# Optimization experiments

Measured on AMD Instinct MI355X. Metric: run time of the kernel, lower is better.

## Reference

```python
import jax, jax.numpy as jnp
import numpy as np

# Model config (matches init_kwargs)
B, S = 4, 1024          # batch of equal-length prefill sequences (cu_seqlens = arange(B+1)*S)
H, KVH, D = 16, 4, 64   # query heads, kv heads (GQA), head_dim
SCALE = 0.125           # 1/sqrt(head_dim)
NUM_SLOTS = 8192        # paged-KV-cache total slots


def setup_inputs() -> dict:
    key = jax.random.key(0)
    k1, k2, k3 = jax.random.split(key, 3)
    N = B * S
    q = jax.random.normal(k1, (N, H * D), dtype=jnp.float32)
    k = jax.random.normal(k2, (N, KVH * D), dtype=jnp.float32)
    v = jax.random.normal(k3, (N, KVH * D), dtype=jnp.float32)
    k_cache = jnp.zeros((NUM_SLOTS, KVH * D), dtype=jnp.float32)
    v_cache = jnp.zeros((NUM_SLOTS, KVH * D), dtype=jnp.float32)
    slot_mapping = jnp.arange(N, dtype=jnp.int32)  # valid slots, no -1 entries
    return {"q": q, "k": k, "v": v, "k_cache": k_cache, "v_cache": v_cache,
            "slot_mapping": slot_mapping}


def _varlen_causal_attn(q, k, v):
    # q: [N, H*D], k/v: [N, KVH*D]; equal-length varlen batch -> [B, S, ...]
    qh = q.reshape(B, S, H, D)
    kh = k.reshape(B, S, KVH, D)
    vh = v.reshape(B, S, KVH, D)
    rep = H // KVH  # GQA: repeat kv heads to match query heads
    kh = jnp.repeat(kh, rep, axis=2)
    vh = jnp.repeat(vh, rep, axis=2)
    scores = jnp.einsum('bqhd,bkhd->bhqk', qh, kh) * SCALE
    causal = jnp.tril(jnp.ones((S, S), dtype=bool))
    scores = jnp.where(causal, scores, jnp.finfo(scores.dtype).min)
    p = jax.nn.softmax(scores, axis=-1)
    o = jnp.einsum('bhqk,bkhd->bqhd', p, vh)
    return o.reshape(B * S, H * D)


def reference(q, k, v, k_cache, v_cache, slot_mapping):
    # store_kvcache: scatter new k/v rows into the paged caches (Triton kernel equivalent)
    k_cache = k_cache.at[slot_mapping].set(k)
    v_cache = v_cache.at[slot_mapping].set(v)
    # prefill path: flash_attn_varlen_func(q, k, v, causal=True) on the fresh k/v
    o = _varlen_causal_attn(q, k, v)
    return o, k_cache, v_cache
```

## Files before the change

kernel.cpp:

```cpp
#include <hip/hip_runtime.h>
#include <hip/hip_bf16.h>

#define B_     4
#define S_     1024
#define H_     16
#define KVH_   4
#define D_     64
#define N_     (B_*S_)
#define SLOTS_ 8192
#define KVD_   (KVH_*D_)
#define HD_    (H_*D_)
#define SCL    (0.125f * 1.44269504f)

#define NATT   1024
#define NCACHE 4096

typedef __attribute__((ext_vector_type(8))) short bf16x8;
typedef __attribute__((ext_vector_type(4))) short bf16x4;
typedef __attribute__((ext_vector_type(4))) float f32x4;

__device__ __forceinline__ short4 f4tob4(float4 f){
    union { __hip_bfloat162 h[2]; short4 s; } u;
    u.h[0] = __float22bfloat162_rn(make_float2(f.x, f.y));
    u.h[1] = __float22bfloat162_rn(make_float2(f.z, f.w));
    return u.s;
}
__device__ __forceinline__ int swz(int row, int col){
    return row*64 + (col ^ ((row & 7) << 3));
}

__global__ void inv_init(int* __restrict__ inv){
    inv[blockIdx.x*256 + threadIdx.x] = -1;
}

__global__ __launch_bounds__(256) void prep_kernel(
    const float* __restrict__ k, const float* __restrict__ v,
    const int* __restrict__ slot_map, int* __restrict__ inv,
    short* __restrict__ Kb, short* __restrict__ Vtb)
{
    const int tid = threadIdx.x;
    if (blockIdx.x >= 256){
        int i = (blockIdx.x - 256)*256 + tid;
        int s = slot_map[i];
        if (s >= 0 && s < SLOTS_) inv[s] = i;
        return;
    }
    __shared__ short sv[64*68];
    const int g   = blockIdx.x >> 4;
    const int s0  = (blockIdx.x & 15) * 64;
    const int b   = g >> 2, kvh = g & 3;

    const int sl = tid >> 2;
    const int cq = (tid & 3) * 16;

    const int n   = b*S_ + s0 + sl;
    const float4* kp = (const float4*)(k + (size_t)n*KVD_ + kvh*D_ + cq);
    const float4* vp = (const float4*)(v + (size_t)n*KVD_ + kvh*D_ + cq);

    float4 kk[4], vv[4];
    #pragma unroll
    for (int j = 0; j < 4; ++j){ kk[j] = kp[j]; vv[j] = vp[j]; }

    short* kbp = Kb + ((size_t)g*S_ + s0 + sl)*64 + cq;
    #pragma unroll
    for (int j = 0; j < 4; ++j)
        *(short4*)(kbp + j*4) = f4tob4(kk[j]);

    #pragma unroll
    for (int j = 0; j < 4; ++j)
        *(short4*)(&sv[sl*68 + cq + j*4]) = f4tob4(vv[j]);
    __syncthreads();

    const int d  = tid >> 2;
    const int sg = (tid & 3) * 16;
    union { short s[16]; bf16x8 v8[2]; } out;
    #pragma unroll
    for (int i = 0; i < 16; ++i)
        out.s[i] = sv[(sg + i)*68 + d];
    short* vtp = Vtb + ((size_t)g*64 + d)*S_ + s0 + sg;
    *(bf16x8*)(vtp)     = out.v8[0];
    *(bf16x8*)(vtp + 8) = out.v8[1];
}

__global__ __launch_bounds__(128, 2) void fused_kernel(
    const float* __restrict__ q, const short* __restrict__ Kb,
    const short* __restrict__ Vtb, float* __restrict__ o,
    const float4* __restrict__ kin, const float4* __restrict__ vin,
    const float4* __restrict__ kcin, const float4* __restrict__ vcin,
    const int* __restrict__ inv,
    float4* __restrict__ kc, float4* __restrict__ vc)
{
    const int tid = threadIdx.x;
    const int bid = blockIdx.x;

    if (bid >= NATT){
        int i = (bid - NATT)*128 + tid;
        int row = i >> 6;
        int n = inv[row];
        if (n >= 0){
            int c = i & 63;
            kc[i] = kin[(size_t)n*64 + c];
            vc[i] = vin[(size_t)n*64 + c];
        } else {
            kc[i] = kcin[i];
            vc[i] = vcin[i];
        }
        return;
    }

    __shared__ __align__(16) short sK[2][64*64];
    __shared__ __align__(16) short sV[2][64*64];

    const int wave = tid >> 6;
    const int lane = tid & 63;
    const int quad = lane >> 4;
    const int l16  = lane & 15;

    const int hp = bid & 1;
    const int g  = (bid >> 1) & 15;
    const int p  = bid >> 5;
    const int qtA = p, qtB = 63 - p;
    const int ntA = (qtA >> 2) + 1;
    const int ntB = (qtB >> 2) + 1;

    const int b = g >> 2, kvh = g & 3;
    const int h = kvh*4 + hp*2 + wave;

    bf16x8 qfA[2], qfB[2];
    {
        const float* qpA = q + ((size_t)(b*S_ + qtA*16 + l16))*HD_ + h*D_ + quad*8;
        const float* qpB = q + ((size_t)(b*S_ + qtB*16 + l16))*HD_ + h*D_ + quad*8;
        #pragma unroll
        for (int ks = 0; ks < 2; ++ks){
            float4 a0 = *(const float4*)(qpA + ks*32);
            float4 a1 = *(const float4*)(qpA + ks*32 + 4);
            float4 b0 = *(const float4*)(qpB + ks*32);
            float4 b1 = *(const float4*)(qpB + ks*32 + 4);
            a0.x*=SCL; a0.y*=SCL; a0.z*=SCL; a0.w*=SCL;
            a1.x*=SCL; a1.y*=SCL; a1.z*=SCL; a1.w*=SCL;
            b0.x*=SCL; b0.y*=SCL; b0.z*=SCL; b0.w*=SCL;
            b1.x*=SCL; b1.y*=SCL; b1.z*=SCL; b1.w*=SCL;
            union { short4 s[2]; bf16x8 v8; } ua, ub;
            ua.s[0] = f4tob4(a0); ua.s[1] = f4tob4(a1);
            ub.s[0] = f4tob4(b0); ub.s[1] = f4tob4(b1);
            qfA[ks] = ua.v8; qfB[ks] = ub.v8;
        }
    }

    f32x4 ofA[4], ofB[4];
    #pragma unroll
    for (int f2 = 0; f2 < 4; ++f2){
        ofA[f2] = (f32x4){0.f,0.f,0.f,0.f};
        ofB[f2] = (f32x4){0.f,0.f,0.f,0.f};
    }
    float lsA = 0.f, lsB = 0.f;
    const int qrowA = qtA*16 + l16, qrowB = qtB*16 + l16;

    const short* Kg = Kb  + (size_t)g*S_*64;
    const short* Vg = Vtb + (size_t)g*64*S_;

    const int rs = tid >> 1;
    const int ch = (tid & 1) * 32;

    bf16x8 kst[4], vst[4];
    #pragma unroll
    for (int j = 0; j < 4; ++j){
        kst[j] = *(const bf16x8*)(Kg + (size_t)rs*64 + ch + j*8);
        vst[j] = *(const bf16x8*)(Vg + (size_t)rs*S_ + ch + j*8);
    }

    for (int t = 0; t < ntB; ++t){
        short* K_ = (short*)sK[t & 1];
        short* V_ = (short*)sV[t & 1];
        #pragma unroll
        for (int j = 0; j < 4; ++j){
            *(bf16x8*)(&K_[swz(rs, ch + j*8)]) = kst[j];
            *(bf16x8*)(&V_[swz(rs, ch + j*8)]) = vst[j];
        }
        if (t + 1 < ntB){
            #pragma unroll
            for (int j = 0; j < 4; ++j){
                kst[j] = *(const bf16x8*)(Kg + (size_t)((t+1)*64 + rs)*64 + ch + j*8);
                vst[j] = *(const bf16x8*)(Vg + (size_t)rs*S_ + (t+1)*64 + ch + j*8);
            }
        }
        __syncthreads();

        const bool actA = (t < ntA);

        bf16x8 kf[2][4];
        #pragma unroll
        for (int ks = 0; ks < 2; ++ks)
            #pragma unroll
            for (int f = 0; f < 4; ++f)
                kf[ks][f] = *(const bf16x8*)(&K_[swz(f*16 + l16, ks*32 + quad*8)]);

        f32x4 scB[4], scA[4];
        #pragma unroll
        for (int f = 0; f < 4; ++f){
            scB[f] = (f32x4){0.f,0.f,0.f,0.f};
            scA[f] = (f32x4){0.f,0.f,0.f,0.f};
        }
        #pragma unroll
        for (int ks = 0; ks < 2; ++ks)
            #pragma unroll
            for (int f = 0; f < 4; ++f)
                scB[f] = __builtin_amdgcn_mfma_f32_16x16x32_bf16(kf[ks][f], qfB[ks], scB[f], 0, 0, 0);
        if (actA){
            #pragma unroll
            for (int ks = 0; ks < 2; ++ks)
                #pragma unroll
                for (int f = 0; f < 4; ++f)
                    scA[f] = __builtin_amdgcn_mfma_f32_16x16x32_bf16(kf[ks][f], qfA[ks], scA[f], 0, 0, 0);
        }

        bf16x4 pfB[4], pfA[4];
        #pragma unroll
        for (int f = 0; f < 4; ++f){
            float4 pf;
            #pragma unroll
            for (int r = 0; r < 4; ++r){
                float pe = __builtin_amdgcn_exp2f(scB[f][r]);
                if (t == ntB - 1 && (t*64 + f*16 + quad*4 + r > qrowB)) pe = 0.f;
                lsB += pe;
                ((float*)&pf)[r] = pe;
            }
            union { short4 s; bf16x4 bv; } u; u.s = f4tob4(pf);
            pfB[f] = u.bv;
        }
        if (actA){
            #pragma unroll
            for (int f = 0; f < 4; ++f){
                float4 pf;
                #pragma unroll
                for (int r = 0; r < 4; ++r){
                    float pe = __builtin_amdgcn_exp2f(scA[f][r]);
                    if (t == ntA - 1 && (t*64 + f*16 + quad*4 + r > qrowA)) pe = 0.f;
                    lsA += pe;
                    ((float*)&pf)[r] = pe;
                }
                union { short4 s; bf16x4 bv; } u; u.s = f4tob4(pf);
                pfA[f] = u.bv;
            }
        }

        #pragma unroll
        for (int f = 0; f < 4; ++f){
            #pragma unroll
            for (int f2 = 0; f2 < 4; ++f2){
                bf16x4 vf = *(const bf16x4*)(&V_[swz(f2*16 + l16, f*16 + quad*4)]);
                ofB[f2] = __builtin_amdgcn_mfma_f32_16x16x16bf16_1k(pfB[f], vf, ofB[f2], 0, 0, 0);
                if (actA)
                    ofA[f2] = __builtin_amdgcn_mfma_f32_16x16x16bf16_1k(pfA[f], vf, ofA[f2], 0, 0, 0);
            }
        }
    }

    auto epilogue = [&](f32x4* of, float lsum, int qt){
        lsum += __shfl_xor(lsum, 16);
        lsum += __shfl_xor(lsum, 32);
        float linv[4];
        #pragma unroll
        for (int r = 0; r < 4; ++r)
            linv[r] = 1.f / __shfl(lsum, quad*4 + r);
        #pragma unroll
        for (int f2 = 0; f2 < 4; ++f2){
            #pragma unroll
            for (int r = 0; r < 4; ++r){
                const int row = qt*16 + quad*4 + r;
                o[((size_t)(b*S_ + row))*HD_ + h*D_ + f2*16 + l16] = of[f2][r] * linv[r];
            }
        }
    };
    epilogue(ofA, lsA, qtA);
    epilogue(ofB, lsB, qtB);
}

extern "C" void kernel_launch(void* const* d_in, const int* in_sizes, int n_in,
                              void* d_out, int out_size, void* d_ws, size_t ws_size,
                              hipStream_t stream){
    (void)in_sizes; (void)n_in; (void)out_size; (void)ws_size;
    const float* q     = (const float*)d_in[0];
    const float* k     = (const float*)d_in[1];
    const float* v     = (const float*)d_in[2];
    const float* kc_in = (const float*)d_in[3];
    const float* vc_in = (const float*)d_in[4];
    const int*   slot  = (const int*)d_in[5];

    float* o  = (float*)d_out;
    float* kc = o + (size_t)N_*HD_;
    float* vc = kc + (size_t)SLOTS_*KVD_;

    short* Kb  = (short*)d_ws;
    short* Vt  = Kb + (size_t)16*S_*64;
    int*   inv = (int*)((char*)d_ws + (4u << 20));

    inv_init<<<SLOTS_/256, 256, 0, stream>>>(inv);

    prep_kernel<<<256 + N_/256, 256, 0, stream>>>(k, v, slot, inv, Kb, Vt);

    fused_kernel<<<NATT + NCACHE, 128, 0, stream>>>(
        q, Kb, Vt, o,
        (const float4*)k, (const float4*)v,
        (const float4*)kc_in, (const float4*)vc_in, inv,
        (float4*)kc, (float4*)vc);
}
```

Baseline: 123.4 us.

## Process two query heads per wave and split cache fill into separate kernel

Each attention wave now handles two query heads of the same GQA group. That halves the attention grid to 512 blocks and doubles reuse of each K/V tile loaded into shared memory. The cache scatter-copy work moves out of the fused kernel into its own launch with 256-thread blocks. This trades fewer blocks and more registers per wave, which risks lower occupancy and fewer blocks than CUs, plus serialising the cache copy behind attention, for halved K/V shared-memory traffic per head.

```diff
diff --git a/kernel.cpp b/kernel.cpp
--- a/kernel.cpp
+++ b/kernel.cpp
@@ -11,9 +11,6 @@
 #define KVD_   (KVH_*D_)
 #define HD_    (H_*D_)
 #define SCL    (0.125f * 1.44269504f)
-
-#define NATT   1024
-#define NCACHE 4096
 
 typedef __attribute__((ext_vector_type(8))) short bf16x8;
 typedef __attribute__((ext_vector_type(4))) short bf16x4;
@@ -82,198 +79,184 @@
     *(bf16x8*)(vtp + 8) = out.v8[1];
 }
 
-__global__ __launch_bounds__(128, 2) void fused_kernel(
+__global__ __launch_bounds__(128, 2) void attn_kernel(
     const float* __restrict__ q, const short* __restrict__ Kb,
-    const short* __restrict__ Vtb, float* __restrict__ o,
+    const short* __restrict__ Vtb, float* __restrict__ o)
+{
+    __shared__ __align__(16) short sK[2][64*64];
+    __shared__ __align__(16) short sV[2][64*64];
+
+    const int tid  = threadIdx.x;
+    const int wave = tid >> 6;
+    const int lane = tid & 63;
+    const int quad = lane >> 4;
+    const int l16  = lane & 15;
+
+    const int g = blockIdx.x & 15;
+    const int p = blockIdx.x >> 4;
+    const int qtA = p, qtB = 63 - p;
+    const int ntA = (qtA >> 2) + 1;
+    const int ntB = (qtB >> 2) + 1;
+
+    const int b = g >> 2, kvh = g & 3;
+    const int h0 = kvh*4 + wave*2;
+
+    bf16x8 qfA[2][2], qfB[2][2];
+    auto load_q = [&](int qt, int h, bf16x8 out[2]){
+        const float* qp = q + ((size_t)(b*S_ + qt*16 + l16))*HD_ + h*D_ + quad*8;
+        #pragma unroll
+        for (int ks = 0; ks < 2; ++ks){
+            float4 a0 = *(const float4*)(qp + ks*32);
+            float4 a1 = *(const float4*)(qp + ks*32 + 4);
+            a0.x*=SCL; a0.y*=SCL; a0.z*=SCL; a0.w*=SCL;
+            a1.x*=SCL; a1.y*=SCL; a1.z*=SCL; a1.w*=SCL;
+            union { short4 s[2]; bf16x8 v8; } u;
+            u.s[0] = f4tob4(a0); u.s[1] = f4tob4(a1);
+            out[ks] = u.v8;
+        }
+    };
+    load_q(qtA, h0,   qfA[0]);
+    load_q(qtA, h0+1, qfA[1]);
+    load_q(qtB, h0,   qfB[0]);
+    load_q(qtB, h0+1, qfB[1]);
+
+    f32x4 ofA[2][4], ofB[2][4];
+    float lsA[2] = {0.f, 0.f}, lsB[2] = {0.f, 0.f};
+    #pragma unroll
+    for (int hh = 0; hh < 2; ++hh)
+        #pragma unroll
+        for (int f2 = 0; f2 < 4; ++f2){
+            ofA[hh][f2] = (f32x4){0.f,0.f,0.f,0.f};
+            ofB[hh][f2] = (f32x4){0.f,0.f,0.f,0.f};
+        }
+    const int qrowA = qtA*16 + l16, qrowB = qtB*16 + l16;
+
+    const short* Kg = Kb  + (size_t)g*S_*64;
+    const short* Vg = Vtb + (size_t)g*64*S_;
+
+    const int rs = tid >> 1;
+    const int ch = (tid & 1) * 32;
+
+    bf16x8 kst[4], vst[4];
+    #pragma unroll
+    for (int j = 0; j < 4; ++j){
+        kst[j] = *(const bf16x8*)(Kg + (size_t)rs*64 + ch + j*8);
+        vst[j] = *(const bf16x8*)(Vg + (size_t)rs*S_ + ch + j*8);
+    }
+
+    for (int t = 0; t < ntB; ++t){
+        short* K_ = (short*)sK[t & 1];
+        short* V_ = (short*)sV[t & 1];
+        #pragma unroll
+        for (int j = 0; j < 4; ++j){
+            *(bf16x8*)(&K_[swz(rs, ch + j*8)]) = kst[j];
+            *(bf16x8*)(&V_[swz(rs, ch + j*8)]) = vst[j];
+        }
+        if (t + 1 < ntB){
+            #pragma unroll
+            for (int j = 0; j < 4; ++j){
+                kst[j] = *(const bf16x8*)(Kg + (size_t)((t+1)*64 + rs)*64 + ch + j*8);
+                vst[j] = *(const bf16x8*)(Vg + (size_t)rs*S_ + (t+1)*64 + ch + j*8);
+            }
+        }
+        __syncthreads();
+
+        const bool actA = (t < ntA);
+
+        bf16x8 kf[2][4];
+        #pragma unroll
+        for (int ks = 0; ks < 2; ++ks)
+            #pragma unroll
+            for (int f = 0; f < 4; ++f)
+                kf[ks][f] = *(const bf16x8*)(&K_[swz(f*16 + l16, ks*32 + quad*8)]);
+
+        auto stream_qk = [&](const bf16x8 qf2[2], float& lsum, bool diag,
+                             int qrow, bf16x4 pf_out[4]){
+            f32x4 sc[4];
+            #pragma unroll
+            for (int f = 0; f < 4; ++f) sc[f] = (f32x4){0.f,0.f,0.f,0.f};
+            #pragma unroll
+            for (int ks = 0; ks < 2; ++ks)
+                #pragma unroll
+                for (int f = 0; f < 4; ++f)
+                    sc[f] = __builtin_amdgcn_mfma_f32_16x16x32_bf16(kf[ks][f], qf2[ks], sc[f], 0, 0, 0);
+            #pragma unroll
+            for (int f = 0; f < 4; ++f){
+                float4 pf;
+                #pragma unroll
+                for (int r = 0; r < 4; ++r){
+                    float pe = __builtin_amdgcn_exp2f(sc[f][r]);
+                    if (diag && (t*64 + f*16 + quad*4 + r > qrow)) pe = 0.f;
+                    lsum += pe;
+                    ((float*)&pf)[r] = pe;
+                }
+                union { short4 s; bf16x4 bv; } u; u.s = f4tob4(pf);
+                pf_out[f] = u.bv;
+            }
+        };
+
+        bf16x4 pB[2][4], pA[2][4];
+        stream_qk(qfB[0], lsB[0], t == ntB - 1, qrowB, pB[0]);
+        stream_qk(qfB[1], lsB[1], t == ntB - 1, qrowB, pB[1]);
+        if (actA){
+            stream_qk(qfA[0], lsA[0], t == ntA - 1, qrowA, pA[0]);
+            stream_qk(qfA[1], lsA[1], t == ntA - 1, qrowA, pA[1]);
+        }
+
+        #pragma unroll
+        for (int f = 0; f < 4; ++f){
+            #pragma unroll
+            for (int f2 = 0; f2 < 4; ++f2){
+                bf16x4 vf = *(const bf16x4*)(&V_[swz(f2*16 + l16, f*16 + quad*4)]);
+                ofB[0][f2] = __builtin_amdgcn_mfma_f32_16x16x16bf16_1k(pB[0][f], vf, ofB[0][f2], 0, 0, 0);
+                ofB[1][f2] = __builtin_amdgcn_mfma_f32_16x16x16bf16_1k(pB[1][f], vf, ofB[1][f2], 0, 0, 0);
+                if (actA){
+                    ofA[0][f2] = __builtin_amdgcn_mfma_f32_16x16x16bf16_1k(pA[0][f], vf, ofA[0][f2], 0, 0, 0);
+                    ofA[1][f2] = __builtin_amdgcn_mfma_f32_16x16x16bf16_1k(pA[1][f], vf, ofA[1][f2], 0, 0, 0);
+                }
+            }
+        }
+    }
+
+    auto epilogue = [&](f32x4* of, float lsum, int qt, int h){
+        lsum += __shfl_xor(lsum, 16);
+        lsum += __shfl_xor(lsum, 32);
+        float linv[4];
+        #pragma unroll
+        for (int r = 0; r < 4; ++r)
+            linv[r] = 1.f / __shfl(lsum, quad*4 + r);
+        #pragma unroll
+        for (int f2 = 0; f2 < 4; ++f2){
+            #pragma unroll
+            for (int r = 0; r < 4; ++r){
+                const int row = qt*16 + quad*4 + r;
+                o[((size_t)(b*S_ + row))*HD_ + h*D_ + f2*16 + l16] = of[f2][r] * linv[r];
+            }
+        }
+    };
+    epilogue(ofA[0], lsA[0], qtA, h0);
+    epilogue(ofA[1], lsA[1], qtA, h0+1);
+    epilogue(ofB[0], lsB[0], qtB, h0);
+    epilogue(ofB[1], lsB[1], qtB, h0+1);
+}
+
+__global__ __launch_bounds__(256) void cache_fill(
     const float4* __restrict__ kin, const float4* __restrict__ vin,
     const float4* __restrict__ kcin, const float4* __restrict__ vcin,
     const int* __restrict__ inv,
     float4* __restrict__ kc, float4* __restrict__ vc)
 {
-    const int tid = threadIdx.x;
-    const int bid = blockIdx.x;
-
-    if (bid >= NATT){
-        int i = (bid - NATT)*128 + tid;
-        int row = i >> 6;
-        int n = inv[row];
-        if (n >= 0){
-            int c = i & 63;
-            kc[i] = kin[(size_t)n*64 + c];
-            vc[i] = vin[(size_t)n*64 + c];
-        } else {
-            kc[i] = kcin[i];
-            vc[i] = vcin[i];
-        }
-        return;
-    }
-
-    __shared__ __align__(16) short sK[2][64*64];
-    __shared__ __align__(16) short sV[2][64*64];
-
-    const int wave = tid >> 6;
-    const int lane = tid & 63;
-    const int quad = lane >> 4;
-    const int l16  = lane & 15;
-
-    const int hp = bid & 1;
-    const int g  = (bid >> 1) & 15;
-    const int p  = bid >> 5;
-    const int qtA = p, qtB = 63 - p;
-    const int ntA = (qtA >> 2) + 1;
-    const int ntB = (qtB >> 2) + 1;
-
-    const int b = g >> 2, kvh = g & 3;
-    const int h = kvh*4 + hp*2 + wave;
-
-    bf16x8 qfA[2], qfB[2];
-    {
-        const float* qpA = q + ((size_t)(b*S_ + qtA*16 + l16))*HD_ + h*D_ + quad*8;
-        const float* qpB = q + ((size_t)(b*S_ + qtB*16 + l16))*HD_ + h*D_ + quad*8;
-        #pragma unroll
-        for (int ks = 0; ks < 2; ++ks){
-            float4 a0 = *(const float4*)(qpA + ks*32);
-            float4 a1 = *(const float4*)(qpA + ks*32 + 4);
-            float4 b0 = *(const float4*)(qpB + ks*32);
-            float4 b1 = *(const float4*)(qpB + ks*32 + 4);
-            a0.x*=SCL; a0.y*=SCL; a0.z*=SCL; a0.w*=SCL;
-            a1.x*=SCL; a1.y*=SCL; a1.z*=SCL; a1.w*=SCL;
-            b0.x*=SCL; b0.y*=SCL; b0.z*=SCL; b0.w*=SCL;
-            b1.x*=SCL; b1.y*=SCL; b1.z*=SCL; b1.w*=SCL;
-            union { short4 s[2]; bf16x8 v8; } ua, ub;
-            ua.s[0] = f4tob4(a0); ua.s[1] = f4tob4(a1);
-            ub.s[0] = f4tob4(b0); ub.s[1] = f4tob4(b1);
-            qfA[ks] = ua.v8; qfB[ks] = ub.v8;
-        }
-    }
-
-    f32x4 ofA[4], ofB[4];
-    #pragma unroll
-    for (int f2 = 0; f2 < 4; ++f2){
-        ofA[f2] = (f32x4){0.f,0.f,0.f,0.f};
-        ofB[f2] = (f32x4){0.f,0.f,0.f,0.f};
-    }
-    float lsA = 0.f, lsB = 0.f;
-    const int qrowA = qtA*16 + l16, qrowB = qtB*16 + l16;
-
-    const short* Kg = Kb  + (size_t)g*S_*64;
-    const short* Vg = Vtb + (size_t)g*64*S_;
-
-    const int rs = tid >> 1;
-    const int ch = (tid & 1) * 32;
-
-    bf16x8 kst[4], vst[4];
-    #pragma unroll
-    for (int j = 0; j < 4; ++j){
-        kst[j] = *(const bf16x8*)(Kg + (size_t)rs*64 + ch + j*8);
-        vst[j] = *(const bf16x8*)(Vg + (size_t)rs*S_ + ch + j*8);
-    }
-
-    for (int t = 0; t < ntB; ++t){
-        short* K_ = (short*)sK[t & 1];
-        short* V_ = (short*)sV[t & 1];
-        #pragma unroll
-        for (int j = 0; j < 4; ++j){
-            *(bf16x8*)(&K_[swz(rs, ch + j*8)]) = kst[j];
-            *(bf16x8*)(&V_[swz(rs, ch + j*8)]) = vst[j];
-        }
-        if (t + 1 < ntB){
-            #pragma unroll
-            for (int j = 0; j < 4; ++j){
-                kst[j] = *(const bf16x8*)(Kg + (size_t)((t+1)*64 + rs)*64 + ch + j*8);
-                vst[j] = *(const bf16x8*)(Vg + (size_t)rs*S_ + (t+1)*64 + ch + j*8);
-            }
-        }
-        __syncthreads();
-
-        const bool actA = (t < ntA);
-
-        bf16x8 kf[2][4];
-        #pragma unroll
-        for (int ks = 0; ks < 2; ++ks)
-            #pragma unroll
-            for (int f = 0; f < 4; ++f)
-                kf[ks][f] = *(const bf16x8*)(&K_[swz(f*16 + l16, ks*32 + quad*8)]);
-
-        f32x4 scB[4], scA[4];
-        #pragma unroll
-        for (int f = 0; f < 4; ++f){
-            scB[f] = (f32x4){0.f,0.f,0.f,0.f};
-            scA[f] = (f32x4){0.f,0.f,0.f,0.f};
-        }
-        #pragma unroll
-        for (int ks = 0; ks < 2; ++ks)
-            #pragma unroll
-            for (int f = 0; f < 4; ++f)
-                scB[f] = __builtin_amdgcn_mfma_f32_16x16x32_bf16(kf[ks][f], qfB[ks], scB[f], 0, 0, 0);
-        if (actA){
-            #pragma unroll
-            for (int ks = 0; ks < 2; ++ks)
-                #pragma unroll
-                for (int f = 0; f < 4; ++f)
-                    scA[f] = __builtin_amdgcn_mfma_f32_16x16x32_bf16(kf[ks][f], qfA[ks], scA[f], 0, 0, 0);
-        }
-
-        bf16x4 pfB[4], pfA[4];
-        #pragma unroll
-        for (int f = 0; f < 4; ++f){
-            float4 pf;
-            #pragma unroll
-            for (int r = 0; r < 4; ++r){
-                float pe = __builtin_amdgcn_exp2f(scB[f][r]);
-                if (t == ntB - 1 && (t*64 + f*16 + quad*4 + r > qrowB)) pe = 0.f;
-                lsB += pe;
-                ((float*)&pf)[r] = pe;
-            }
-            union { short4 s; bf16x4 bv; } u; u.s = f4tob4(pf);
-            pfB[f] = u.bv;
-        }
-        if (actA){
-            #pragma unroll
-            for (int f = 0; f < 4; ++f){
-                float4 pf;
-                #pragma unroll
-                for (int r = 0; r < 4; ++r){
-                    float pe = __builtin_amdgcn_exp2f(scA[f][r]);
-                    if (t == ntA - 1 && (t*64 + f*16 + quad*4 + r > qrowA)) pe = 0.f;
-                    lsA += pe;
-                    ((float*)&pf)[r] = pe;
-                }
-                union { short4 s; bf16x4 bv; } u; u.s = f4tob4(pf);
-                pfA[f] = u.bv;
-            }
-        }
-
-        #pragma unroll
-        for (int f = 0; f < 4; ++f){
-            #pragma unroll
-            for (int f2 = 0; f2 < 4; ++f2){
-                bf16x4 vf = *(const bf16x4*)(&V_[swz(f2*16 + l16, f*16 + quad*4)]);
-                ofB[f2] = __builtin_amdgcn_mfma_f32_16x16x16bf16_1k(pfB[f], vf, ofB[f2], 0, 0, 0);
-                if (actA)
-                    ofA[f2] = __builtin_amdgcn_mfma_f32_16x16x16bf16_1k(pfA[f], vf, ofA[f2], 0, 0, 0);
-            }
-        }
-    }
-
-    auto epilogue = [&](f32x4* of, float lsum, int qt){
-        lsum += __shfl_xor(lsum, 16);
-        lsum += __shfl_xor(lsum, 32);
-        float linv[4];
-        #pragma unroll
-        for (int r = 0; r < 4; ++r)
-            linv[r] = 1.f / __shfl(lsum, quad*4 + r);
-        #pragma unroll
-        for (int f2 = 0; f2 < 4; ++f2){
-            #pragma unroll
-            for (int r = 0; r < 4; ++r){
-                const int row = qt*16 + quad*4 + r;
-                o[((size_t)(b*S_ + row))*HD_ + h*D_ + f2*16 + l16] = of[f2][r] * linv[r];
-            }
-        }
-    };
-    epilogue(ofA, lsA, qtA);
-    epilogue(ofB, lsB, qtB);
+    int i = blockIdx.x*256 + threadIdx.x;
+    int row = i >> 6;
+    int n = inv[row];
+    if (n >= 0){
+        int c = i & 63;
+        kc[i] = kin[(size_t)n*64 + c];
+        vc[i] = vin[(size_t)n*64 + c];
+    } else {
+        kc[i] = kcin[i];
+        vc[i] = vcin[i];
+    }
 }
 
 extern "C" void kernel_launch(void* const* d_in, const int* in_sizes, int n_in,
@@ -299,8 +282,9 @@
 
     prep_kernel<<<256 + N_/256, 256, 0, stream>>>(k, v, slot, inv, Kb, Vt);
 
-    fused_kernel<<<NATT + NCACHE, 128, 0, stream>>>(
-        q, Kb, Vt, o,
+    attn_kernel<<<512, 128, 0, stream>>>(q, Kb, Vt, o);
+
+    cache_fill<<<(SLOTS_*64)/256, 256, 0, stream>>>(
         (const float4*)k, (const float4*)v,
         (const float4*)kc_in, (const float4*)vc_in, inv,
         (float4*)kc, (float4*)vc);
```

Result: slower. 129.6 us (+5.1%).

## Split cache fill into separate kernel and use 4-wave blocks covering all GQA heads

Applied to the files above, without the earlier changes.

The attention kernel now runs 256-thread blocks where four waves handle all four query heads sharing one KV head. Each staged K/V tile is therefore reused by twice as many waves, and the grid halves to 512 blocks. The cache-scatter work moves out of the fused grid into its own kernel launched afterwards. This cuts shared-memory staging traffic per head, but adds a kernel launch, serializes the cache copy after attention instead of overlapping it, and lowers the number of blocks available for load balancing.

```diff
diff --git a/kernel.cpp b/kernel.cpp
--- a/kernel.cpp
+++ b/kernel.cpp
@@ -11,9 +11,6 @@
 #define KVD_   (KVH_*D_)
 #define HD_    (H_*D_)
 #define SCL    (0.125f * 1.44269504f)
-
-#define NATT   1024
-#define NCACHE 4096
 
 typedef __attribute__((ext_vector_type(8))) short bf16x8;
 typedef __attribute__((ext_vector_type(4))) short bf16x4;
@@ -82,49 +79,27 @@
     *(bf16x8*)(vtp + 8) = out.v8[1];
 }
 
-__global__ __launch_bounds__(128, 2) void fused_kernel(
+__global__ __launch_bounds__(256, 2) void attn_kernel(
     const float* __restrict__ q, const short* __restrict__ Kb,
-    const short* __restrict__ Vtb, float* __restrict__ o,
-    const float4* __restrict__ kin, const float4* __restrict__ vin,
-    const float4* __restrict__ kcin, const float4* __restrict__ vcin,
-    const int* __restrict__ inv,
-    float4* __restrict__ kc, float4* __restrict__ vc)
+    const short* __restrict__ Vtb, float* __restrict__ o)
 {
-    const int tid = threadIdx.x;
-    const int bid = blockIdx.x;
-
-    if (bid >= NATT){
-        int i = (bid - NATT)*128 + tid;
-        int row = i >> 6;
-        int n = inv[row];
-        if (n >= 0){
-            int c = i & 63;
-            kc[i] = kin[(size_t)n*64 + c];
-            vc[i] = vin[(size_t)n*64 + c];
-        } else {
-            kc[i] = kcin[i];
-            vc[i] = vcin[i];
-        }
-        return;
-    }
-
     __shared__ __align__(16) short sK[2][64*64];
     __shared__ __align__(16) short sV[2][64*64];
 
+    const int tid  = threadIdx.x;
     const int wave = tid >> 6;
     const int lane = tid & 63;
     const int quad = lane >> 4;
     const int l16  = lane & 15;
 
-    const int hp = bid & 1;
-    const int g  = (bid >> 1) & 15;
-    const int p  = bid >> 5;
+    const int g = blockIdx.x & 15;
+    const int p = blockIdx.x >> 4;
     const int qtA = p, qtB = 63 - p;
     const int ntA = (qtA >> 2) + 1;
     const int ntB = (qtB >> 2) + 1;
 
     const int b = g >> 2, kvh = g & 3;
-    const int h = kvh*4 + hp*2 + wave;
+    const int h = kvh*4 + wave;
 
     bf16x8 qfA[2], qfB[2];
     {
@@ -159,30 +134,27 @@
     const short* Kg = Kb  + (size_t)g*S_*64;
     const short* Vg = Vtb + (size_t)g*64*S_;
 
-    const int rs = tid >> 1;
-    const int ch = (tid & 1) * 32;
-
-    bf16x8 kst[4], vst[4];
-    #pragma unroll
-    for (int j = 0; j < 4; ++j){
-        kst[j] = *(const bf16x8*)(Kg + (size_t)rs*64 + ch + j*8);
-        vst[j] = *(const bf16x8*)(Vg + (size_t)rs*S_ + ch + j*8);
-    }
+    const int rs = tid >> 2;
+    const int cg = (tid & 3) * 16;
+
+    bf16x8 kst[2], vst[2];
+    kst[0] = *(const bf16x8*)(Kg + (size_t)rs*64 + cg);
+    kst[1] = *(const bf16x8*)(Kg + (size_t)rs*64 + cg + 8);
+    vst[0] = *(const bf16x8*)(Vg + (size_t)rs*S_ + cg);
+    vst[1] = *(const bf16x8*)(Vg + (size_t)rs*S_ + cg + 8);
 
     for (int t = 0; t < ntB; ++t){
         short* K_ = (short*)sK[t & 1];
         short* V_ = (short*)sV[t & 1];
-        #pragma unroll
-        for (int j = 0; j < 4; ++j){
-            *(bf16x8*)(&K_[swz(rs, ch + j*8)]) = kst[j];
-            *(bf16x8*)(&V_[swz(rs, ch + j*8)]) = vst[j];
-        }
+        *(bf16x8*)(&K_[swz(rs, cg)])     = kst[0];
+        *(bf16x8*)(&K_[swz(rs, cg + 8)]) = kst[1];
+        *(bf16x8*)(&V_[swz(rs, cg)])     = vst[0];
+        *(bf16x8*)(&V_[swz(rs, cg + 8)]) = vst[1];
         if (t + 1 < ntB){
-            #pragma unroll
-            for (int j = 0; j < 4; ++j){
-                kst[j] = *(const bf16x8*)(Kg + (size_t)((t+1)*64 + rs)*64 + ch + j*8);
-                vst[j] = *(const bf16x8*)(Vg + (size_t)rs*S_ + (t+1)*64 + ch + j*8);
-            }
+            kst[0] = *(const bf16x8*)(Kg + (size_t)((t+1)*64 + rs)*64 + cg);
+            kst[1] = *(const bf16x8*)(Kg + (size_t)((t+1)*64 + rs)*64 + cg + 8);
+            vst[0] = *(const bf16x8*)(Vg + (size_t)rs*S_ + (t+1)*64 + cg);
+            vst[1] = *(const bf16x8*)(Vg + (size_t)rs*S_ + (t+1)*64 + cg + 8);
         }
         __syncthreads();
 
@@ -214,7 +186,7 @@
                     scA[f] = __builtin_amdgcn_mfma_f32_16x16x32_bf16(kf[ks][f], qfA[ks], scA[f], 0, 0, 0);
         }
 
-        bf16x4 pfB[4], pfA[4];
+        bf16x4 pB[4], pA[4];
         #pragma unroll
         for (int f = 0; f < 4; ++f){
             float4 pf;
@@ -226,7 +198,7 @@
                 ((float*)&pf)[r] = pe;
             }
             union { short4 s; bf16x4 bv; } u; u.s = f4tob4(pf);
-            pfB[f] = u.bv;
+            pB[f] = u.bv;
         }
         if (actA){
             #pragma unroll
@@ -240,7 +212,7 @@
                     ((float*)&pf)[r] = pe;
                 }
                 union { short4 s; bf16x4 bv; } u; u.s = f4tob4(pf);
-                pfA[f] = u.bv;
+                pA[f] = u.bv;
             }
         }
 
@@ -249,9 +221,9 @@
             #pragma unroll
             for (int f2 = 0; f2 < 4; ++f2){
                 bf16x4 vf = *(const bf16x4*)(&V_[swz(f2*16 + l16, f*16 + quad*4)]);
-                ofB[f2] = __builtin_amdgcn_mfma_f32_16x16x16bf16_1k(pfB[f], vf, ofB[f2], 0, 0, 0);
+                ofB[f2] = __builtin_amdgcn_mfma_f32_16x16x16bf16_1k(pB[f], vf, ofB[f2], 0, 0, 0);
                 if (actA)
-                    ofA[f2] = __builtin_amdgcn_mfma_f32_16x16x16bf16_1k(pfA[f], vf, ofA[f2], 0, 0, 0);
+                    ofA[f2] = __builtin_amdgcn_mfma_f32_16x16x16bf16_1k(pA[f], vf, ofA[f2], 0, 0, 0);
             }
         }
     }
@@ -274,6 +246,25 @@
     };
     epilogue(ofA, lsA, qtA);
     epilogue(ofB, lsB, qtB);
+}
+
+__global__ __launch_bounds__(256) void cache_fill(
+    const float4* __restrict__ kin, const float4* __restrict__ vin,
+    const float4* __restrict__ kcin, const float4* __restrict__ vcin,
+    const int* __restrict__ inv,
+    float4* __restrict__ kc, float4* __restrict__ vc)
+{
+    int i = blockIdx.x*256 + threadIdx.x;
+    int row = i >> 6;
+    int n = inv[row];
+    if (n >= 0){
+        int c = i & 63;
+        kc[i] = kin[(size_t)n*64 + c];
+        vc[i] = vin[(size_t)n*64 + c];
+    } else {
+        kc[i] = kcin[i];
+        vc[i] = vcin[i];
+    }
 }
 
 extern "C" void kernel_launch(void* const* d_in, const int* in_sizes, int n_in,
@@ -299,8 +290,9 @@
 
     prep_kernel<<<256 + N_/256, 256, 0, stream>>>(k, v, slot, inv, Kb, Vt);
 
-    fused_kernel<<<NATT + NCACHE, 128, 0, stream>>>(
-        q, Kb, Vt, o,
+    attn_kernel<<<512, 256, 0, stream>>>(q, Kb, Vt, o);
+
+    cache_fill<<<(SLOTS_*64)/256, 256, 0, stream>>>(
         (const float4*)k, (const float4*)v,
         (const float4*)kc_in, (const float4*)vc_in, inv,
         (float4*)kc, (float4*)vc);
```

After: 127.3 us. +3.2%, slower.
